# Kernel optimization log

Measured on AMD Instinct MI355X. Metric: run time of the kernel, lower is better.

The kernel has to match this reference:

```python
import jax, jax.numpy as jnp
import numpy as np

N_NODES = 100000
N_EDGES = 1600000
D_IN = 128
D_HID = 128
D_OUT = 64


def _glorot(key, shape):
    lim = float(np.sqrt(6.0 / (shape[0] + shape[1])))
    return jax.random.uniform(key, shape, jnp.float32, -lim, lim)


def setup_inputs() -> dict:
    key = jax.random.key(0)
    ks = jax.random.split(key, 8)
    x = jax.random.normal(ks[0], (N_NODES, D_IN), jnp.float32)
    edge_index = jax.random.randint(ks[1], (2, N_EDGES), 0, N_NODES, jnp.int64)
    # SAGEConv layer 0: in=128 -> out=128 (lin_l with bias on aggregated, lin_r no bias on root)
    W_l0 = _glorot(ks[2], (D_IN, D_HID))
    b_l0 = jnp.zeros((D_HID,), jnp.float32)
    W_r0 = _glorot(ks[3], (D_IN, D_HID))
    # SAGEConv layer 1: in=128 -> out=64
    W_l1 = _glorot(ks[4], (D_HID, D_OUT))
    b_l1 = jnp.zeros((D_OUT,), jnp.float32)
    W_r1 = _glorot(ks[5], (D_HID, D_OUT))
    return {"x": x, "edge_index": edge_index,
            "W_l0": W_l0, "b_l0": b_l0, "W_r0": W_r0,
            "W_l1": W_l1, "b_l1": b_l1, "W_r1": W_r1}


def _sage_conv(x, src, dst, W_l, b_l, W_r):
    # mean aggregation of source features at targets (PyG SAGEConv default aggr='mean')
    msgs = x[src]                                              # [E, d_in] irregular gather
    agg = jax.ops.segment_sum(msgs, dst, num_segments=N_NODES)  # [N, d_in]
    cnt = jax.ops.segment_sum(jnp.ones((src.shape[0],), x.dtype), dst,
                              num_segments=N_NODES)            # [N]
    mean = agg / jnp.maximum(cnt, 1.0)[:, None]
    return mean @ W_l + b_l + x @ W_r


def reference(x, edge_index, W_l0, b_l0, W_r0, W_l1, b_l1, W_r1):
    src, dst = edge_index[0], edge_index[1]
    h = _sage_conv(x, src, dst, W_l0, b_l0, W_r0)
    h = jax.nn.relu(h)
    # dropout is identity at inference (training=False)
    out = _sage_conv(h, src, dst, W_l1, b_l1, W_r1)
    return out
```

## Files before the change

### kernel.cpp

```cpp
#include <hip/hip_runtime.h>
#include <type_traits>

#define NN 100000
#define NE 1600000
#define DF 128
#define NBKT 196
#define BKT_SHIFT 9
#define EPB 6250

typedef unsigned short ushort_t;
typedef unsigned int uint_t;
typedef __bf16 bf16x8 __attribute__((ext_vector_type(8)));
typedef float f32x4 __attribute__((ext_vector_type(4)));

union ABFrag { uint4 u; bf16x8 v; ushort_t s[8]; };

__device__ __forceinline__ float bf2f(ushort_t u) {
    uint_t v = ((uint_t)u) << 16;
    float f;
    __builtin_memcpy(&f, &v, 4);
    return f;
}

__device__ __forceinline__ ushort_t f2bf(float f) {
    uint_t u;
    __builtin_memcpy(&u, &f, 4);
    uint_t rounding = 0x7FFFu + ((u >> 16) & 1u);
    u += rounding;
    return (ushort_t)(u >> 16);
}

__global__ void k_detect(const int* ei, int* flag) {
    int l = threadIdx.x;
    int v = ei[l];
    bool ok = ((l & 1) == 0) || (v == 0);
    unsigned long long m = __ballot(ok);
    if (l == 0) flag[0] = (m == 0xFFFFFFFFFFFFFFFFULL) ? 1 : 0;
}

__global__ __launch_bounds__(256) void k_bktcnt(const int* __restrict__ ei,
                                                const int* __restrict__ flag,
                                                int* __restrict__ M) {
    __shared__ int cnt[NBKT];
    int t = threadIdx.x, blk = blockIdx.x;
    for (int i = t; i < NBKT; i += 256) cnt[i] = 0;
    __syncthreads();
    int e0 = blk * EPB;
    if (flag[0]) {
        const long long* p = (const long long*)ei;
        for (int i = t; i < EPB; i += 256) {
            int d = (int)p[(size_t)NE + e0 + i];
            atomicAdd(&cnt[d >> BKT_SHIFT], 1);
        }
    } else {
        for (int i = t; i < EPB; i += 256) {
            int d = ei[NE + e0 + i];
            atomicAdd(&cnt[d >> BKT_SHIFT], 1);
        }
    }
    __syncthreads();
    for (int i = t; i < NBKT; i += 256) M[i * 256 + blk] = cnt[i];
}

__global__ __launch_bounds__(256) void k_colscan(int* __restrict__ M, int* __restrict__ colsum) {
    __shared__ int sm[256];
    int t = threadIdx.x, b = blockIdx.x;
    int v = M[b * 256 + t];
    sm[t] = v;
    __syncthreads();
    for (int o = 1; o < 256; o <<= 1) {
        int add = (t >= o) ? sm[t - o] : 0;
        __syncthreads();
        sm[t] += add;
        __syncthreads();
    }
    M[b * 256 + t] = sm[t] - v;
    if (t == 255) colsum[b] = sm[255];
}

__global__ __launch_bounds__(256) void k_bktscan(const int* __restrict__ colsum,
                                                 int* __restrict__ bkbase, int* __restrict__ rs) {
    __shared__ int sm[256];
    int t = threadIdx.x;
    int v = (t < NBKT) ? colsum[t] : 0;
    sm[t] = v;
    __syncthreads();
    for (int o = 1; o < 256; o <<= 1) {
        int add = (t >= o) ? sm[t - o] : 0;
        __syncthreads();
        sm[t] += add;
        __syncthreads();
    }
    if (t <= NBKT) bkbase[t] = sm[t] - v;
    if (t == 0) rs[NN] = NE;
}

__global__ __launch_bounds__(256) void k_bktscatter(const int* __restrict__ ei,
                                                    const int* __restrict__ flag,
                                                    const int* __restrict__ M,
                                                    const int* __restrict__ bkbase,
                                                    uint2* __restrict__ tmp) {
    __shared__ int cur[NBKT];
    int t = threadIdx.x, blk = blockIdx.x;
    for (int i = t; i < NBKT; i += 256) cur[i] = bkbase[i] + M[i * 256 + blk];
    __syncthreads();
    int e0 = blk * EPB;
    if (flag[0]) {
        const long long* p = (const long long*)ei;
        for (int i = t; i < EPB; i += 256) {
            int e = e0 + i;
            int s = (int)p[e], d = (int)p[(size_t)NE + e];
            int pos = atomicAdd(&cur[d >> BKT_SHIFT], 1);
            tmp[pos] = make_uint2((uint_t)s, (uint_t)d);
        }
    } else {
        for (int i = t; i < EPB; i += 256) {
            int e = e0 + i;
            int s = ei[e], d = ei[NE + e];
            int pos = atomicAdd(&cur[d >> BKT_SHIFT], 1);
            tmp[pos] = make_uint2((uint_t)s, (uint_t)d);
        }
    }
}

__global__ __launch_bounds__(256) void k_bktsort(const uint2* __restrict__ tmp,
                                                 const int* __restrict__ bkbase,
                                                 int* __restrict__ rs, int* __restrict__ esrc) {
    __shared__ int hist[512];
    __shared__ int curp[512];
    int t = threadIdx.x, b = blockIdx.x;
    int nbase = b << BKT_SHIFT;
    int bb = bkbase[b], be = bkbase[b + 1];
    hist[t] = 0;
    hist[t + 256] = 0;
    __syncthreads();
    for (int i = bb + t; i < be; i += 256)
        atomicAdd(&hist[(int)tmp[i].y - nbase], 1);
    __syncthreads();
    int ov0 = hist[t], ov1 = hist[t + 256];
    for (int o = 1; o < 512; o <<= 1) {
        int v0 = (t >= o) ? hist[t - o] : 0;
        int v1 = (t + 256 >= o) ? hist[t + 256 - o] : 0;
        __syncthreads();
        hist[t] += v0;
        hist[t + 256] += v1;
        __syncthreads();
    }
    int ex0 = bb + hist[t] - ov0;
    int ex1 = bb + hist[t + 256] - ov1;
    int n0 = nbase + t, n1 = nbase + t + 256;
    if (n0 < NN) rs[n0] = ex0;
    if (n1 < NN) rs[n1] = ex1;
    curp[t] = ex0;
    curp[t + 256] = ex1;
    __syncthreads();
    for (int i = bb + t; i < be; i += 256) {
        uint2 pr = tmp[i];
        int pos = atomicAdd(&curp[(int)pr.y - nbase], 1);
        esrc[pos] = (int)pr.x;
    }
}

__global__ void k_cast(const float* __restrict__ src, ushort_t* __restrict__ dst, int n4) {
    int i = blockIdx.x * 256 + threadIdx.x;
    if (i < n4) {
        float4 f = ((const float4*)src)[i];
        uint2 o;
        o.x = (uint_t)f2bf(f.x) | ((uint_t)f2bf(f.y) << 16);
        o.y = (uint_t)f2bf(f.z) | ((uint_t)f2bf(f.w) << 16);
        ((uint2*)dst)[i] = o;
    }
}

__global__ void k_packW(const float* Wl, const float* Wr, ushort_t* dst, int NT) {
    int NC = NT * 16;
    int total = 8 * NT * 512;
    int idx = blockIdx.x * 256 + threadIdx.x;
    if (idx >= total) return;
    int j = idx & 7;
    int lane = (idx >> 3) & 63;
    int rem = idx / 512;
    int t = rem % NT;
    int s = rem / NT;
    int quad = lane >> 4, l16 = lane & 15;
    int k = (s & 3) * 32 + quad * 8 + j;
    int n = t * 16 + l16;
    const float* W = (s < 4) ? Wl : Wr;
    dst[idx] = f2bf(W[k * NC + n]);
}

__global__ __launch_bounds__(256) void k_agg(const ushort_t* __restrict__ feat,
                                             const int* __restrict__ rs,
                                             const int* __restrict__ esrc,
                                             ushort_t* __restrict__ outm) {
    int wv = threadIdx.x >> 6;
    int lane = threadIdx.x & 63;
    int n = blockIdx.x * 4 + wv;
    if (n >= NN) return;
    int s0 = rs[n], s1 = rs[n + 1];
    float a0 = 0.f, a1 = 0.f;
    for (int base = s0; base < s1; base += 64) {
        int c = s1 - base;
        if (c > 64) c = 64;
        int my = (lane < c) ? esrc[base + lane] : 0;
        int e = 0;
        for (; e + 4 <= c; e += 4) {
            int r0 = __shfl(my, e);
            int r1 = __shfl(my, e + 1);
            int r2 = __shfl(my, e + 2);
            int r3 = __shfl(my, e + 3);
            uint_t v0 = *(const uint_t*)(feat + (size_t)r0 * DF + lane * 2);
            uint_t v1 = *(const uint_t*)(feat + (size_t)r1 * DF + lane * 2);
            uint_t v2 = *(const uint_t*)(feat + (size_t)r2 * DF + lane * 2);
            uint_t v3 = *(const uint_t*)(feat + (size_t)r3 * DF + lane * 2);
            a0 += bf2f((ushort_t)(v0 & 0xffff)) + bf2f((ushort_t)(v1 & 0xffff)) +
                  bf2f((ushort_t)(v2 & 0xffff)) + bf2f((ushort_t)(v3 & 0xffff));
            a1 += bf2f((ushort_t)(v0 >> 16)) + bf2f((ushort_t)(v1 >> 16)) +
                  bf2f((ushort_t)(v2 >> 16)) + bf2f((ushort_t)(v3 >> 16));
        }
        for (; e < c; ++e) {
            int r = __shfl(my, e);
            uint_t v = *(const uint_t*)(feat + (size_t)r * DF + lane * 2);
            a0 += bf2f((ushort_t)(v & 0xffff));
            a1 += bf2f((ushort_t)(v >> 16));
        }
    }
    int deg = s1 - s0;
    float inv = 1.0f / (float)(deg > 0 ? deg : 1);
    a0 *= inv;
    a1 *= inv;
    uint_t o = (uint_t)f2bf(a0) | ((uint_t)f2bf(a1) << 16);
    *(uint_t*)(outm + (size_t)n * DF + lane * 2) = o;
}

template <int NT, bool RELU, typename OutT>
__global__ __launch_bounds__(256) void k_gemm(const ushort_t* __restrict__ A0,
                                              const ushort_t* __restrict__ A1,
                                              const ushort_t* __restrict__ Wpk,
                                              const float* __restrict__ bias,
                                              OutT* __restrict__ out) {
    const int NC = NT * 16;
    int warp = threadIdx.x >> 6;
    int lane = threadIdx.x & 63;
    int quad = lane >> 4;
    int l16 = lane & 15;
    int m0 = blockIdx.x * 64 + warp * 16;

    int rowA = m0 + l16;
    if (rowA >= NN) rowA = NN - 1;
    const int kofs = quad * 8;

    f32x4 acc[NT];
#pragma unroll
    for (int t = 0; t < NT; t++) acc[t] = (f32x4){0.f, 0.f, 0.f, 0.f};

#pragma unroll
    for (int s = 0; s < 8; s++) {
        const ushort_t* Ab = (s < 4) ? A0 : A1;
        int kk = (s & 3) * 32 + kofs;
        ABFrag a;
        a.u = *(const uint4*)(Ab + (size_t)rowA * DF + kk);
#pragma unroll
        for (int t = 0; t < NT; t++) {
            ABFrag b;
            b.u = *(const uint4*)(Wpk + ((size_t)(s * NT + t) * 64 + lane) * 8);
            acc[t] = __builtin_amdgcn_mfma_f32_16x16x32_bf16(a.v, b.v, acc[t], 0, 0, 0);
        }
    }

#pragma unroll
    for (int t = 0; t < NT; t++) {
        int col = t * 16 + l16;
        float bv = bias[col];
#pragma unroll
        for (int r = 0; r < 4; r++) {
            int row = m0 + quad * 4 + r;
            if (row < NN) {
                float v = acc[t][r] + bv;
                if (RELU) v = fmaxf(v, 0.f);
                if constexpr (std::is_same<OutT, ushort_t>::value)
                    out[(size_t)row * NC + col] = f2bf(v);
                else
                    out[(size_t)row * NC + col] = v;
            }
        }
    }
}

extern "C" void kernel_launch(void* const* d_in, const int* in_sizes, int n_in,
                              void* d_out, int out_size, void* d_ws, size_t ws_size,
                              hipStream_t stream) {
    const float* x   = (const float*)d_in[0];
    const int*   ei  = (const int*)d_in[1];
    const float* Wl0 = (const float*)d_in[2];
    const float* bl0 = (const float*)d_in[3];
    const float* Wr0 = (const float*)d_in[4];
    const float* Wl1 = (const float*)d_in[5];
    const float* bl1 = (const float*)d_in[6];
    const float* Wr1 = (const float*)d_in[7];
    float* out = (float*)d_out;

    char* ws = (char*)d_ws;
    size_t off = 0;
    auto alloc = [&](size_t b) {
        size_t o = off;
        off += (b + 255) & ~(size_t)255;
        return o;
    };
    int* flag   = (int*)(ws + alloc(64));
    int* rs     = (int*)(ws + alloc((size_t)(NN + 1) * 4));
    int* M      = (int*)(ws + alloc((size_t)NBKT * 256 * 4));
    int* colsum = (int*)(ws + alloc((size_t)NBKT * 4));
    int* bkbase = (int*)(ws + alloc((size_t)(NBKT + 1) * 4));
    int* esrc   = (int*)(ws + alloc((size_t)NE * 4));
    ushort_t* pw0  = (ushort_t*)(ws + alloc((size_t)8 * 8 * 512 * 2));
    ushort_t* pw1  = (ushort_t*)(ws + alloc((size_t)8 * 4 * 512 * 2));
    ushort_t* xb   = (ushort_t*)(ws + alloc((size_t)NN * DF * 2));
    ushort_t* mean = (ushort_t*)(ws + alloc((size_t)NN * DF * 2));
    ushort_t* h    = (ushort_t*)(ws + alloc((size_t)NN * DF * 2));
    uint2* tmp = (uint2*)mean;

    const int N4 = NN * DF / 4;

    k_detect<<<1, 64, 0, stream>>>(ei, flag);
    k_bktcnt<<<256, 256, 0, stream>>>(ei, flag, M);
    k_colscan<<<NBKT, 256, 0, stream>>>(M, colsum);
    k_bktscan<<<1, 256, 0, stream>>>(colsum, bkbase, rs);
    k_bktscatter<<<256, 256, 0, stream>>>(ei, flag, M, bkbase, tmp);
    k_bktsort<<<NBKT, 256, 0, stream>>>(tmp, bkbase, rs, esrc);
    k_cast<<<(N4 + 255) / 256, 256, 0, stream>>>(x, xb, N4);
    k_packW<<<(8 * 8 * 512 + 255) / 256, 256, 0, stream>>>(Wl0, Wr0, pw0, 8);
    k_packW<<<(8 * 4 * 512 + 255) / 256, 256, 0, stream>>>(Wl1, Wr1, pw1, 4);

    k_agg<<<NN / 4, 256, 0, stream>>>(xb, rs, esrc, mean);
    k_gemm<8, true, ushort_t><<<(NN + 63) / 64, 256, 0, stream>>>(mean, xb, pw0, bl0, h);
    k_agg<<<NN / 4, 256, 0, stream>>>(h, rs, esrc, mean);
    k_gemm<4, false, float><<<(NN + 63) / 64, 256, 0, stream>>>(mean, h, pw1, bl1, out);
}
```

Baseline: 332.1 us.

## Transform before aggregating in layer 2 and vectorize neighbor gathers

Layer 2 now applies the linear maps first, using the identity mean(h)@W_l = mean(h@W_l). The neighbor projection is written as a 64-wide bf16 buffer and the root projection plus bias as fp32, so the gather moves 64 features per edge instead of 128. Both aggregation kernels now place several nodes in one wavefront and read 16-byte vectors per lane. A zero sentinel row at index NN lets padded lanes run without branching. The cost is extra launches and sentinel/zero-row bookkeeping, plus wasted lanes when node degrees within a wave differ.

```diff
diff --git a/kernel.cpp b/kernel.cpp
--- a/kernel.cpp
+++ b/kernel.cpp
@@ -15,19 +15,17 @@
 
 union ABFrag { uint4 u; bf16x8 v; ushort_t s[8]; };
 
-__device__ __forceinline__ float bf2f(ushort_t u) {
-    uint_t v = ((uint_t)u) << 16;
-    float f;
-    __builtin_memcpy(&f, &v, 4);
-    return f;
-}
-
 __device__ __forceinline__ ushort_t f2bf(float f) {
     uint_t u;
     __builtin_memcpy(&u, &f, 4);
     uint_t rounding = 0x7FFFu + ((u >> 16) & 1u);
     u += rounding;
     return (ushort_t)(u >> 16);
+}
+__device__ __forceinline__ float lo_f(uint_t u) { return __uint_as_float(u << 16); }
+__device__ __forceinline__ float hi_f(uint_t u) { return __uint_as_float(u & 0xffff0000u); }
+__device__ __forceinline__ uint_t pack2(float a, float b) {
+    return (uint_t)f2bf(a) | ((uint_t)f2bf(b) << 16);
 }
 
 __global__ void k_detect(const int* ei, int* flag) {
@@ -166,71 +164,191 @@
     if (i < n4) {
         float4 f = ((const float4*)src)[i];
         uint2 o;
-        o.x = (uint_t)f2bf(f.x) | ((uint_t)f2bf(f.y) << 16);
-        o.y = (uint_t)f2bf(f.z) | ((uint_t)f2bf(f.w) << 16);
+        o.x = pack2(f.x, f.y);
+        o.y = pack2(f.z, f.w);
         ((uint2*)dst)[i] = o;
-    }
-}
-
-__global__ void k_packW(const float* Wl, const float* Wr, ushort_t* dst, int NT) {
-    int NC = NT * 16;
-    int total = 8 * NT * 512;
+    } else if (i < n4 + 32) {
+        ((uint2*)dst)[i] = make_uint2(0u, 0u);
+    }
+}
+
+__global__ void k_packW0(const float* Wl, const float* Wr, ushort_t* dst) {
+    int total = 8 * 8 * 512;
     int idx = blockIdx.x * 256 + threadIdx.x;
     if (idx >= total) return;
     int j = idx & 7;
     int lane = (idx >> 3) & 63;
     int rem = idx / 512;
-    int t = rem % NT;
-    int s = rem / NT;
+    int t = rem % 8;
+    int s = rem / 8;
     int quad = lane >> 4, l16 = lane & 15;
     int k = (s & 3) * 32 + quad * 8 + j;
     int n = t * 16 + l16;
     const float* W = (s < 4) ? Wl : Wr;
-    dst[idx] = f2bf(W[k * NC + n]);
-}
-
-__global__ __launch_bounds__(256) void k_agg(const ushort_t* __restrict__ feat,
-                                             const int* __restrict__ rs,
-                                             const int* __restrict__ esrc,
-                                             ushort_t* __restrict__ outm) {
+    dst[idx] = f2bf(W[k * 128 + n]);
+}
+
+__global__ void k_packW1(const float* Wl, const float* Wr, ushort_t* dst) {
+    int total = 4 * 8 * 512;
+    int idx = blockIdx.x * 256 + threadIdx.x;
+    if (idx >= total) return;
+    int j = idx & 7;
+    int lane = (idx >> 3) & 63;
+    int rem = idx / 512;
+    int t = rem % 8;
+    int s = rem / 8;
+    int quad = lane >> 4, l16 = lane & 15;
+    int k = s * 32 + quad * 8 + j;
+    int n = (t & 3) * 16 + l16;
+    const float* W = (t < 4) ? Wl : Wr;
+    dst[idx] = f2bf(W[k * 64 + n]);
+}
+
+__global__ void k_zrow2(ushort_t* tbuf) {
+    int t = threadIdx.x;
+    if (t < 32) ((uint_t*)(tbuf + (size_t)NN * 64))[t] = 0u;
+}
+
+__global__ __launch_bounds__(256) void k_agg0(const ushort_t* __restrict__ feat,
+                                              const int* __restrict__ rs,
+                                              const int* __restrict__ esrc,
+                                              ushort_t* __restrict__ outm) {
     int wv = threadIdx.x >> 6;
     int lane = threadIdx.x & 63;
-    int n = blockIdx.x * 4 + wv;
-    if (n >= NN) return;
-    int s0 = rs[n], s1 = rs[n + 1];
-    float a0 = 0.f, a1 = 0.f;
-    for (int base = s0; base < s1; base += 64) {
-        int c = s1 - base;
-        if (c > 64) c = 64;
-        int my = (lane < c) ? esrc[base + lane] : 0;
+    int li = lane & 15;
+    int gbase = lane & 48;
+    int n = (blockIdx.x * 4 + wv) * 4 + (lane >> 4);
+    int s0 = 0, deg = 0;
+    if (n < NN) {
+        s0 = rs[n];
+        deg = rs[n + 1] - s0;
+    }
+    int md = deg;
+    md = max(md, __shfl_xor(md, 16));
+    md = max(md, __shfl_xor(md, 32));
+    float acc[8] = {0.f, 0.f, 0.f, 0.f, 0.f, 0.f, 0.f, 0.f};
+    const ushort_t* fb = feat + li * 8;
+    int clampIdx = (deg > 0) ? deg - 1 : 0;
+    for (int c = 0; c < md; c += 16) {
+        int ii = c + li;
+        if (ii > clampIdx) ii = clampIdx;
+        int my = esrc[s0 + ii];
+        int lim = md - c;
+        if (lim > 16) lim = 16;
         int e = 0;
-        for (; e + 4 <= c; e += 4) {
-            int r0 = __shfl(my, e);
-            int r1 = __shfl(my, e + 1);
-            int r2 = __shfl(my, e + 2);
-            int r3 = __shfl(my, e + 3);
-            uint_t v0 = *(const uint_t*)(feat + (size_t)r0 * DF + lane * 2);
-            uint_t v1 = *(const uint_t*)(feat + (size_t)r1 * DF + lane * 2);
-            uint_t v2 = *(const uint_t*)(feat + (size_t)r2 * DF + lane * 2);
-            uint_t v3 = *(const uint_t*)(feat + (size_t)r3 * DF + lane * 2);
-            a0 += bf2f((ushort_t)(v0 & 0xffff)) + bf2f((ushort_t)(v1 & 0xffff)) +
-                  bf2f((ushort_t)(v2 & 0xffff)) + bf2f((ushort_t)(v3 & 0xffff));
-            a1 += bf2f((ushort_t)(v0 >> 16)) + bf2f((ushort_t)(v1 >> 16)) +
-                  bf2f((ushort_t)(v2 >> 16)) + bf2f((ushort_t)(v3 >> 16));
-        }
-        for (; e < c; ++e) {
-            int r = __shfl(my, e);
-            uint_t v = *(const uint_t*)(feat + (size_t)r * DF + lane * 2);
-            a0 += bf2f((ushort_t)(v & 0xffff));
-            a1 += bf2f((ushort_t)(v >> 16));
-        }
-    }
-    int deg = s1 - s0;
-    float inv = 1.0f / (float)(deg > 0 ? deg : 1);
-    a0 *= inv;
-    a1 *= inv;
-    uint_t o = (uint_t)f2bf(a0) | ((uint_t)f2bf(a1) << 16);
-    *(uint_t*)(outm + (size_t)n * DF + lane * 2) = o;
+        for (; e + 4 <= lim; e += 4) {
+            int r0 = __shfl(my, gbase + e);
+            int r1 = __shfl(my, gbase + e + 1);
+            int r2 = __shfl(my, gbase + e + 2);
+            int r3 = __shfl(my, gbase + e + 3);
+            r0 = (c + e < deg) ? r0 : NN;
+            r1 = (c + e + 1 < deg) ? r1 : NN;
+            r2 = (c + e + 2 < deg) ? r2 : NN;
+            r3 = (c + e + 3 < deg) ? r3 : NN;
+            uint4 v0 = *(const uint4*)(fb + (size_t)r0 * DF);
+            uint4 v1 = *(const uint4*)(fb + (size_t)r1 * DF);
+            uint4 v2 = *(const uint4*)(fb + (size_t)r2 * DF);
+            uint4 v3 = *(const uint4*)(fb + (size_t)r3 * DF);
+            acc[0] += lo_f(v0.x); acc[1] += hi_f(v0.x); acc[2] += lo_f(v0.y); acc[3] += hi_f(v0.y);
+            acc[4] += lo_f(v0.z); acc[5] += hi_f(v0.z); acc[6] += lo_f(v0.w); acc[7] += hi_f(v0.w);
+            acc[0] += lo_f(v1.x); acc[1] += hi_f(v1.x); acc[2] += lo_f(v1.y); acc[3] += hi_f(v1.y);
+            acc[4] += lo_f(v1.z); acc[5] += hi_f(v1.z); acc[6] += lo_f(v1.w); acc[7] += hi_f(v1.w);
+            acc[0] += lo_f(v2.x); acc[1] += hi_f(v2.x); acc[2] += lo_f(v2.y); acc[3] += hi_f(v2.y);
+            acc[4] += lo_f(v2.z); acc[5] += hi_f(v2.z); acc[6] += lo_f(v2.w); acc[7] += hi_f(v2.w);
+            acc[0] += lo_f(v3.x); acc[1] += hi_f(v3.x); acc[2] += lo_f(v3.y); acc[3] += hi_f(v3.y);
+            acc[4] += lo_f(v3.z); acc[5] += hi_f(v3.z); acc[6] += lo_f(v3.w); acc[7] += hi_f(v3.w);
+        }
+        for (; e < lim; ++e) {
+            int r = __shfl(my, gbase + e);
+            r = (c + e < deg) ? r : NN;
+            uint4 v = *(const uint4*)(fb + (size_t)r * DF);
+            acc[0] += lo_f(v.x); acc[1] += hi_f(v.x); acc[2] += lo_f(v.y); acc[3] += hi_f(v.y);
+            acc[4] += lo_f(v.z); acc[5] += hi_f(v.z); acc[6] += lo_f(v.w); acc[7] += hi_f(v.w);
+        }
+    }
+    if (n < NN) {
+        float inv = 1.0f / (float)(deg > 0 ? deg : 1);
+        uint4 o;
+        o.x = pack2(acc[0] * inv, acc[1] * inv);
+        o.y = pack2(acc[2] * inv, acc[3] * inv);
+        o.z = pack2(acc[4] * inv, acc[5] * inv);
+        o.w = pack2(acc[6] * inv, acc[7] * inv);
+        *(uint4*)(outm + (size_t)n * DF + li * 8) = o;
+    }
+}
+
+__global__ __launch_bounds__(256) void k_agg2(const ushort_t* __restrict__ tbuf,
+                                              const float* __restrict__ rbuf,
+                                              const int* __restrict__ rs,
+                                              const int* __restrict__ esrc,
+                                              float* __restrict__ out) {
+    int wv = threadIdx.x >> 6;
+    int lane = threadIdx.x & 63;
+    int li = lane & 7;
+    int gbase = lane & 56;
+    int n = (blockIdx.x * 4 + wv) * 8 + (lane >> 3);
+    int s0 = 0, deg = 0;
+    if (n < NN) {
+        s0 = rs[n];
+        deg = rs[n + 1] - s0;
+    }
+    int md = deg;
+    md = max(md, __shfl_xor(md, 8));
+    md = max(md, __shfl_xor(md, 16));
+    md = max(md, __shfl_xor(md, 32));
+    float acc[8] = {0.f, 0.f, 0.f, 0.f, 0.f, 0.f, 0.f, 0.f};
+    const ushort_t* fb = tbuf + li * 8;
+    int clampIdx = (deg > 0) ? deg - 1 : 0;
+    for (int c = 0; c < md; c += 8) {
+        int ii = c + li;
+        if (ii > clampIdx) ii = clampIdx;
+        int my = esrc[s0 + ii];
+        int lim = md - c;
+        if (lim > 8) lim = 8;
+        int e = 0;
+        for (; e + 4 <= lim; e += 4) {
+            int r0 = __shfl(my, gbase + e);
+            int r1 = __shfl(my, gbase + e + 1);
+            int r2 = __shfl(my, gbase + e + 2);
+            int r3 = __shfl(my, gbase + e + 3);
+            r0 = (c + e < deg) ? r0 : NN;
+            r1 = (c + e + 1 < deg) ? r1 : NN;
+            r2 = (c + e + 2 < deg) ? r2 : NN;
+            r3 = (c + e + 3 < deg) ? r3 : NN;
+            uint4 v0 = *(const uint4*)(fb + (size_t)r0 * 64);
+            uint4 v1 = *(const uint4*)(fb + (size_t)r1 * 64);
+            uint4 v2 = *(const uint4*)(fb + (size_t)r2 * 64);
+            uint4 v3 = *(const uint4*)(fb + (size_t)r3 * 64);
+            acc[0] += lo_f(v0.x); acc[1] += hi_f(v0.x); acc[2] += lo_f(v0.y); acc[3] += hi_f(v0.y);
+            acc[4] += lo_f(v0.z); acc[5] += hi_f(v0.z); acc[6] += lo_f(v0.w); acc[7] += hi_f(v0.w);
+            acc[0] += lo_f(v1.x); acc[1] += hi_f(v1.x); acc[2] += lo_f(v1.y); acc[3] += hi_f(v1.y);
+            acc[4] += lo_f(v1.z); acc[5] += hi_f(v1.z); acc[6] += lo_f(v1.w); acc[7] += hi_f(v1.w);
+            acc[0] += lo_f(v2.x); acc[1] += hi_f(v2.x); acc[2] += lo_f(v2.y); acc[3] += hi_f(v2.y);
+            acc[4] += lo_f(v2.z); acc[5] += hi_f(v2.z); acc[6] += lo_f(v2.w); acc[7] += hi_f(v2.w);
+            acc[0] += lo_f(v3.x); acc[1] += hi_f(v3.x); acc[2] += lo_f(v3.y); acc[3] += hi_f(v3.y);
+            acc[4] += lo_f(v3.z); acc[5] += hi_f(v3.z); acc[6] += lo_f(v3.w); acc[7] += hi_f(v3.w);
+        }
+        for (; e < lim; ++e) {
+            int r = __shfl(my, gbase + e);
+            r = (c + e < deg) ? r : NN;
+            uint4 v = *(const uint4*)(fb + (size_t)r * 64);
+            acc[0] += lo_f(v.x); acc[1] += hi_f(v.x); acc[2] += lo_f(v.y); acc[3] += hi_f(v.y);
+            acc[4] += lo_f(v.z); acc[5] += hi_f(v.z); acc[6] += lo_f(v.w); acc[7] += hi_f(v.w);
+        }
+    }
+    if (n < NN) {
+        float inv = 1.0f / (float)(deg > 0 ? deg : 1);
+        const float4* rp = (const float4*)(rbuf + (size_t)n * 64 + li * 8);
+        float4 ra = rp[0], rb = rp[1];
+        float4 oa, ob;
+        oa.x = acc[0] * inv + ra.x; oa.y = acc[1] * inv + ra.y;
+        oa.z = acc[2] * inv + ra.z; oa.w = acc[3] * inv + ra.w;
+        ob.x = acc[4] * inv + rb.x; ob.y = acc[5] * inv + rb.y;
+        ob.z = acc[6] * inv + rb.z; ob.w = acc[7] * inv + rb.w;
+        float4* op = (float4*)(out + (size_t)n * 64 + li * 8);
+        op[0] = oa;
+        op[1] = ob;
+    }
 }
 
 template <int NT, bool RELU, typename OutT>
@@ -282,6 +400,56 @@
                     out[(size_t)row * NC + col] = f2bf(v);
                 else
                     out[(size_t)row * NC + col] = v;
+            }
+        }
+    }
+}
+
+__global__ __launch_bounds__(256) void k_gemm2(const ushort_t* __restrict__ A,
+                                               const ushort_t* __restrict__ Wpk,
+                                               const float* __restrict__ bias,
+                                               ushort_t* __restrict__ tbuf,
+                                               float* __restrict__ rbuf) {
+    int warp = threadIdx.x >> 6;
+    int lane = threadIdx.x & 63;
+    int quad = lane >> 4;
+    int l16 = lane & 15;
+    int m0 = blockIdx.x * 64 + warp * 16;
+
+    int rowA = m0 + l16;
+    if (rowA >= NN) rowA = NN - 1;
+    const int kofs = quad * 8;
+
+    f32x4 acc[8];
+#pragma unroll
+    for (int t = 0; t < 8; t++) acc[t] = (f32x4){0.f, 0.f, 0.f, 0.f};
+
+#pragma unroll
+    for (int s = 0; s < 4; s++) {
+        int kk = s * 32 + kofs;
+        ABFrag a;
+        a.u = *(const uint4*)(A + (size_t)rowA * DF + kk);
+#pragma unroll
+        for (int t = 0; t < 8; t++) {
+            ABFrag b;
+            b.u = *(const uint4*)(Wpk + ((size_t)(s * 8 + t) * 64 + lane) * 8);
+            acc[t] = __builtin_amdgcn_mfma_f32_16x16x32_bf16(a.v, b.v, acc[t], 0, 0, 0);
+        }
+    }
+
+#pragma unroll
+    for (int t = 0; t < 8; t++) {
+        int cc = (t & 3) * 16 + l16;
+        float bv = (t >= 4) ? bias[cc] : 0.f;
+#pragma unroll
+        for (int r = 0; r < 4; r++) {
+            int row = m0 + quad * 4 + r;
+            if (row < NN) {
+                float v = acc[t][r];
+                if (t < 4)
+                    tbuf[(size_t)row * 64 + cc] = f2bf(v);
+                else
+                    rbuf[(size_t)row * 64 + cc] = v + bv;
             }
         }
     }
@@ -314,11 +482,13 @@
     int* bkbase = (int*)(ws + alloc((size_t)(NBKT + 1) * 4));
     int* esrc   = (int*)(ws + alloc((size_t)NE * 4));
     ushort_t* pw0  = (ushort_t*)(ws + alloc((size_t)8 * 8 * 512 * 2));
-    ushort_t* pw1  = (ushort_t*)(ws + alloc((size_t)8 * 4 * 512 * 2));
-    ushort_t* xb   = (ushort_t*)(ws + alloc((size_t)NN * DF * 2));
+    ushort_t* pw1  = (ushort_t*)(ws + alloc((size_t)4 * 8 * 512 * 2));
+    ushort_t* xb   = (ushort_t*)(ws + alloc((size_t)(NN + 1) * DF * 2));
     ushort_t* mean = (ushort_t*)(ws + alloc((size_t)NN * DF * 2));
     ushort_t* h    = (ushort_t*)(ws + alloc((size_t)NN * DF * 2));
     uint2* tmp = (uint2*)mean;
+    ushort_t* tbuf = xb;
+    float* rbuf = (float*)mean;
 
     const int N4 = NN * DF / 4;
 
@@ -328,12 +498,13 @@
     k_bktscan<<<1, 256, 0, stream>>>(colsum, bkbase, rs);
     k_bktscatter<<<256, 256, 0, stream>>>(ei, flag, M, bkbase, tmp);
     k_bktsort<<<NBKT, 256, 0, stream>>>(tmp, bkbase, rs, esrc);
-    k_cast<<<(N4 + 255) / 256, 256, 0, stream>>>(x, xb, N4);
-    k_packW<<<(8 * 8 * 512 + 255) / 256, 256, 0, stream>>>(Wl0, Wr0, pw0, 8);
-    k_packW<<<(8 * 4 * 512 + 255) / 256, 256, 0, stream>>>(Wl1, Wr1, pw1, 4);
-
-    k_agg<<<NN / 4, 256, 0, stream>>>(xb, rs, esrc, mean);
+    k_cast<<<(N4 + 32 + 255) / 256, 256, 0, stream>>>(x, xb, N4);
+    k_packW0<<<(8 * 8 * 512 + 255) / 256, 256, 0, stream>>>(Wl0, Wr0, pw0);
+    k_packW1<<<(4 * 8 * 512 + 255) / 256, 256, 0, stream>>>(Wl1, Wr1, pw1);
+
+    k_agg0<<<NN / 16, 256, 0, stream>>>(xb, rs, esrc, mean);
     k_gemm<8, true, ushort_t><<<(NN + 63) / 64, 256, 0, stream>>>(mean, xb, pw0, bl0, h);
-    k_agg<<<NN / 4, 256, 0, stream>>>(h, rs, esrc, mean);
-    k_gemm<4, false, float><<<(NN + 63) / 64, 256, 0, stream>>>(mean, h, pw1, bl1, out);
-}
+    k_gemm2<<<(NN + 63) / 64, 256, 0, stream>>>(h, pw1, bl1, tbuf, rbuf);
+    k_zrow2<<<1, 64, 0, stream>>>(tbuf);
+    k_agg2<<<(NN + 31) / 32, 256, 0, stream>>>(tbuf, rbuf, rs, esrc, out);
+}
```

Measured after the change: 310.6 us. -6.5%, faster.

## Fuse layer-0 aggregation and both GEMMs, aggregate projected layer-1 features

Applied to the files above, without the earlier changes.

Uses linearity of mean aggregation to project h by W_l1 before gathering, so the second aggregation gathers 64-wide bf16 rows instead of 128-wide ones. Layer-0 aggregation, the layer-0 GEMM with ReLU and the layer-1 projections are fused into one kernel through LDS, so mean and h never round-trip through global memory. The new gathers use 16-byte loads with a zero sentinel row in place of divergent tails. Format detection is folded into the sort kernels and the cast and pack kernels are merged, cutting launches. Rounding the projected features to bf16 before aggregation slightly changes numerics.

```diff
diff --git a/kernel.cpp b/kernel.cpp
--- a/kernel.cpp
+++ b/kernel.cpp
@@ -15,13 +15,6 @@
 
 union ABFrag { uint4 u; bf16x8 v; ushort_t s[8]; };
 
-__device__ __forceinline__ float bf2f(ushort_t u) {
-    uint_t v = ((uint_t)u) << 16;
-    float f;
-    __builtin_memcpy(&f, &v, 4);
-    return f;
-}
-
 __device__ __forceinline__ ushort_t f2bf(float f) {
     uint_t u;
     __builtin_memcpy(&u, &f, 4);
@@ -29,24 +22,33 @@
     u += rounding;
     return (ushort_t)(u >> 16);
 }
-
-__global__ void k_detect(const int* ei, int* flag) {
-    int l = threadIdx.x;
-    int v = ei[l];
-    bool ok = ((l & 1) == 0) || (v == 0);
-    unsigned long long m = __ballot(ok);
-    if (l == 0) flag[0] = (m == 0xFFFFFFFFFFFFFFFFULL) ? 1 : 0;
+__device__ __forceinline__ float lo_f(uint_t u) { return __uint_as_float(u << 16); }
+__device__ __forceinline__ float hi_f(uint_t u) { return __uint_as_float(u & 0xffff0000u); }
+__device__ __forceinline__ uint_t pack2(float a, float b) {
+    return (uint_t)f2bf(a) | ((uint_t)f2bf(b) << 16);
+}
+
+__device__ __forceinline__ int detect64(const int* ei, int* s64) {
+    if (threadIdx.x < 64) {
+        int v = ei[threadIdx.x];
+        bool ok = ((threadIdx.x & 1) == 0) || (v == 0);
+        unsigned long long m = __ballot(ok);
+        if (threadIdx.x == 0) *s64 = (m == 0xFFFFFFFFFFFFFFFFULL) ? 1 : 0;
+    }
+    __syncthreads();
+    return *s64;
 }
 
 __global__ __launch_bounds__(256) void k_bktcnt(const int* __restrict__ ei,
-                                                const int* __restrict__ flag,
                                                 int* __restrict__ M) {
     __shared__ int cnt[NBKT];
+    __shared__ int s64;
     int t = threadIdx.x, blk = blockIdx.x;
+    int is64 = detect64(ei, &s64);
     for (int i = t; i < NBKT; i += 256) cnt[i] = 0;
     __syncthreads();
     int e0 = blk * EPB;
-    if (flag[0]) {
+    if (is64) {
         const long long* p = (const long long*)ei;
         for (int i = t; i < EPB; i += 256) {
             int d = (int)p[(size_t)NE + e0 + i];
@@ -96,16 +98,17 @@
 }
 
 __global__ __launch_bounds__(256) void k_bktscatter(const int* __restrict__ ei,
-                                                    const int* __restrict__ flag,
                                                     const int* __restrict__ M,
                                                     const int* __restrict__ bkbase,
                                                     uint2* __restrict__ tmp) {
     __shared__ int cur[NBKT];
+    __shared__ int s64;
     int t = threadIdx.x, blk = blockIdx.x;
+    int is64 = detect64(ei, &s64);
     for (int i = t; i < NBKT; i += 256) cur[i] = bkbase[i] + M[i * 256 + blk];
     __syncthreads();
     int e0 = blk * EPB;
-    if (flag[0]) {
+    if (is64) {
         const long long* p = (const long long*)ei;
         for (int i = t; i < EPB; i += 256) {
             int e = e0 + i;
@@ -161,130 +164,217 @@
     }
 }
 
-__global__ void k_cast(const float* __restrict__ src, ushort_t* __restrict__ dst, int n4) {
-    int i = blockIdx.x * 256 + threadIdx.x;
-    if (i < n4) {
-        float4 f = ((const float4*)src)[i];
-        uint2 o;
-        o.x = (uint_t)f2bf(f.x) | ((uint_t)f2bf(f.y) << 16);
-        o.y = (uint_t)f2bf(f.z) | ((uint_t)f2bf(f.w) << 16);
-        ((uint2*)dst)[i] = o;
-    }
-}
-
-__global__ void k_packW(const float* Wl, const float* Wr, ushort_t* dst, int NT) {
-    int NC = NT * 16;
-    int total = 8 * NT * 512;
-    int idx = blockIdx.x * 256 + threadIdx.x;
-    if (idx >= total) return;
-    int j = idx & 7;
-    int lane = (idx >> 3) & 63;
-    int rem = idx / 512;
-    int t = rem % NT;
-    int s = rem / NT;
-    int quad = lane >> 4, l16 = lane & 15;
-    int k = (s & 3) * 32 + quad * 8 + j;
-    int n = t * 16 + l16;
-    const float* W = (s < 4) ? Wl : Wr;
-    dst[idx] = f2bf(W[k * NC + n]);
-}
-
-__global__ __launch_bounds__(256) void k_agg(const ushort_t* __restrict__ feat,
-                                             const int* __restrict__ rs,
-                                             const int* __restrict__ esrc,
-                                             ushort_t* __restrict__ outm) {
+#define CAST_B 12501
+__global__ void k_prep(const float* __restrict__ x, ushort_t* __restrict__ xb,
+                       const float* __restrict__ Wl0, const float* __restrict__ Wr0,
+                       ushort_t* __restrict__ pw0,
+                       const float* __restrict__ Wl1, const float* __restrict__ Wr1,
+                       ushort_t* __restrict__ pw1) {
+    const int n4 = NN * DF / 4;
+    int blk = blockIdx.x, t = threadIdx.x;
+    if (blk < CAST_B) {
+        int i = blk * 256 + t;
+        if (i < n4) {
+            float4 f = ((const float4*)x)[i];
+            uint2 o;
+            o.x = pack2(f.x, f.y);
+            o.y = pack2(f.z, f.w);
+            ((uint2*)xb)[i] = o;
+        } else if (i < n4 + 32) {
+            ((uint2*)xb)[i] = make_uint2(0u, 0u);
+        }
+    } else if (blk < CAST_B + 128) {
+        int idx = (blk - CAST_B) * 256 + t;
+        int j = idx & 7;
+        int lane = (idx >> 3) & 63;
+        int rem = idx / 512;
+        int tt = rem % 8;
+        int s = rem / 8;
+        int quad = lane >> 4, l16 = lane & 15;
+        int k = (s & 3) * 32 + quad * 8 + j;
+        int n = tt * 16 + l16;
+        const float* W = (s < 4) ? Wl0 : Wr0;
+        pw0[idx] = f2bf(W[k * 128 + n]);
+    } else {
+        int idx = (blk - CAST_B - 128) * 256 + t;
+        int j = idx & 7;
+        int lane = (idx >> 3) & 63;
+        int rem = idx / 512;
+        int tt = rem % 8;
+        int s = rem / 8;
+        int quad = lane >> 4, l16 = lane & 15;
+        int k = s * 32 + quad * 8 + j;
+        int n = (tt & 3) * 16 + l16;
+        const float* W = (tt < 4) ? Wl1 : Wr1;
+        pw1[idx] = f2bf(W[k * 64 + n]);
+    }
+}
+
+__global__ __launch_bounds__(256) void k_fused(const ushort_t* __restrict__ xb,
+                                               const int* __restrict__ rs,
+                                               const int* __restrict__ esrc,
+                                               const ushort_t* __restrict__ pw0,
+                                               const float* __restrict__ bl0,
+                                               const ushort_t* __restrict__ pw1,
+                                               const float* __restrict__ bl1,
+                                               ushort_t* __restrict__ tbuf,
+                                               float* __restrict__ rbuf) {
+    __shared__ ushort_t m_lds[16][136];
+    __shared__ ushort_t h_lds[16][136];
+    int tid = threadIdx.x;
+    int wv = tid >> 6, lane = tid & 63;
+    int l16 = lane & 15, quad = lane >> 4, gbase = lane & 48;
+    int n0 = blockIdx.x * 16;
+
+    int n = n0 + wv * 4 + quad;
+    int s0 = rs[n];
+    int deg = rs[n + 1] - s0;
+    int md = deg;
+    md = max(md, __shfl_xor(md, 16));
+    md = max(md, __shfl_xor(md, 32));
+    float acc[8] = {0.f, 0.f, 0.f, 0.f, 0.f, 0.f, 0.f, 0.f};
+    const ushort_t* fb = xb + l16 * 8;
+    int clampIdx = (deg > 0) ? deg - 1 : 0;
+    for (int c = 0; c < md; c += 16) {
+        int ii = c + l16;
+        if (ii > clampIdx) ii = clampIdx;
+        int my = esrc[s0 + ii];
+        uint4 v[16];
+#pragma unroll
+        for (int e = 0; e < 16; e++) {
+            int r = __shfl(my, gbase + e);
+            r = (c + e < deg) ? r : NN;
+            v[e] = *(const uint4*)(fb + (size_t)r * DF);
+        }
+#pragma unroll
+        for (int e = 0; e < 16; e++) {
+            acc[0] += lo_f(v[e].x); acc[1] += hi_f(v[e].x);
+            acc[2] += lo_f(v[e].y); acc[3] += hi_f(v[e].y);
+            acc[4] += lo_f(v[e].z); acc[5] += hi_f(v[e].z);
+            acc[6] += lo_f(v[e].w); acc[7] += hi_f(v[e].w);
+        }
+    }
+    {
+        float inv = 1.0f / (float)(deg > 0 ? deg : 1);
+        int nl = wv * 4 + quad;
+        uint_t* mp = (uint_t*)&m_lds[nl][l16 * 8];
+        mp[0] = pack2(acc[0] * inv, acc[1] * inv);
+        mp[1] = pack2(acc[2] * inv, acc[3] * inv);
+        mp[2] = pack2(acc[4] * inv, acc[5] * inv);
+        mp[3] = pack2(acc[6] * inv, acc[7] * inv);
+    }
+    __syncthreads();
+
+    const int kofs = quad * 8;
+    f32x4 c0[2] = {(f32x4){0.f, 0.f, 0.f, 0.f}, (f32x4){0.f, 0.f, 0.f, 0.f}};
+#pragma unroll
+    for (int s = 0; s < 8; s++) {
+        ABFrag a;
+        if (s < 4)
+            a.u = *(const uint4*)&m_lds[l16][(s & 3) * 32 + kofs];
+        else
+            a.u = *(const uint4*)(xb + (size_t)(n0 + l16) * DF + (s & 3) * 32 + kofs);
+#pragma unroll
+        for (int i = 0; i < 2; i++) {
+            int t = wv * 2 + i;
+            ABFrag b;
+            b.u = *(const uint4*)(pw0 + ((size_t)(s * 8 + t) * 64 + lane) * 8);
+            c0[i] = __builtin_amdgcn_mfma_f32_16x16x32_bf16(a.v, b.v, c0[i], 0, 0, 0);
+        }
+    }
+#pragma unroll
+    for (int i = 0; i < 2; i++) {
+        int col = wv * 32 + i * 16 + l16;
+        float bv = bl0[col];
+#pragma unroll
+        for (int r = 0; r < 4; r++) {
+            float v = fmaxf(c0[i][r] + bv, 0.f);
+            h_lds[quad * 4 + r][col] = f2bf(v);
+        }
+    }
+    __syncthreads();
+
+    f32x4 c1[2] = {(f32x4){0.f, 0.f, 0.f, 0.f}, (f32x4){0.f, 0.f, 0.f, 0.f}};
+#pragma unroll
+    for (int s = 0; s < 4; s++) {
+        ABFrag a;
+        a.u = *(const uint4*)&h_lds[l16][s * 32 + kofs];
+#pragma unroll
+        for (int i = 0; i < 2; i++) {
+            int t = wv * 2 + i;
+            ABFrag b;
+            b.u = *(const uint4*)(pw1 + ((size_t)(s * 8 + t) * 64 + lane) * 8);
+            c1[i] = __builtin_amdgcn_mfma_f32_16x16x32_bf16(a.v, b.v, c1[i], 0, 0, 0);
+        }
+    }
+#pragma unroll
+    for (int i = 0; i < 2; i++) {
+        int t = wv * 2 + i;
+        int cc = (t & 3) * 16 + l16;
+        if (t < 4) {
+#pragma unroll
+            for (int r = 0; r < 4; r++)
+                tbuf[(size_t)(n0 + quad * 4 + r) * 64 + cc] = f2bf(c1[i][r]);
+        } else {
+            float bv = bl1[cc];
+#pragma unroll
+            for (int r = 0; r < 4; r++)
+                rbuf[(size_t)(n0 + quad * 4 + r) * 64 + cc] = c1[i][r] + bv;
+        }
+    }
+    if (blockIdx.x == 0 && tid < 32)
+        ((uint_t*)(tbuf + (size_t)NN * 64))[tid] = 0u;
+}
+
+__global__ __launch_bounds__(256) void k_agg2(const ushort_t* __restrict__ tbuf,
+                                              const float* __restrict__ rbuf,
+                                              const int* __restrict__ rs,
+                                              const int* __restrict__ esrc,
+                                              float* __restrict__ out) {
     int wv = threadIdx.x >> 6;
     int lane = threadIdx.x & 63;
-    int n = blockIdx.x * 4 + wv;
-    if (n >= NN) return;
-    int s0 = rs[n], s1 = rs[n + 1];
-    float a0 = 0.f, a1 = 0.f;
-    for (int base = s0; base < s1; base += 64) {
-        int c = s1 - base;
-        if (c > 64) c = 64;
-        int my = (lane < c) ? esrc[base + lane] : 0;
-        int e = 0;
-        for (; e + 4 <= c; e += 4) {
-            int r0 = __shfl(my, e);
-            int r1 = __shfl(my, e + 1);
-            int r2 = __shfl(my, e + 2);
-            int r3 = __shfl(my, e + 3);
-            uint_t v0 = *(const uint_t*)(feat + (size_t)r0 * DF + lane * 2);
-            uint_t v1 = *(const uint_t*)(feat + (size_t)r1 * DF + lane * 2);
-            uint_t v2 = *(const uint_t*)(feat + (size_t)r2 * DF + lane * 2);
-            uint_t v3 = *(const uint_t*)(feat + (size_t)r3 * DF + lane * 2);
-            a0 += bf2f((ushort_t)(v0 & 0xffff)) + bf2f((ushort_t)(v1 & 0xffff)) +
-                  bf2f((ushort_t)(v2 & 0xffff)) + bf2f((ushort_t)(v3 & 0xffff));
-            a1 += bf2f((ushort_t)(v0 >> 16)) + bf2f((ushort_t)(v1 >> 16)) +
-                  bf2f((ushort_t)(v2 >> 16)) + bf2f((ushort_t)(v3 >> 16));
-        }
-        for (; e < c; ++e) {
-            int r = __shfl(my, e);
-            uint_t v = *(const uint_t*)(feat + (size_t)r * DF + lane * 2);
-            a0 += bf2f((ushort_t)(v & 0xffff));
-            a1 += bf2f((ushort_t)(v >> 16));
-        }
-    }
-    int deg = s1 - s0;
+    int li = lane & 7;
+    int gbase = lane & 56;
+    int n = (blockIdx.x * 4 + wv) * 8 + (lane >> 3);
+    int s0 = rs[n];
+    int deg = rs[n + 1] - s0;
+    int md = deg;
+    md = max(md, __shfl_xor(md, 8));
+    md = max(md, __shfl_xor(md, 16));
+    md = max(md, __shfl_xor(md, 32));
+    float acc[8] = {0.f, 0.f, 0.f, 0.f, 0.f, 0.f, 0.f, 0.f};
+    const ushort_t* fb = tbuf + li * 8;
+    int clampIdx = (deg > 0) ? deg - 1 : 0;
+    for (int c = 0; c < md; c += 8) {
+        int ii = c + li;
+        if (ii > clampIdx) ii = clampIdx;
+        int my = esrc[s0 + ii];
+        uint4 v[8];
+#pragma unroll
+        for (int e = 0; e < 8; e++) {
+            int r = __shfl(my, gbase + e);
+            r = (c + e < deg) ? r : NN;
+            v[e] = *(const uint4*)(fb + (size_t)r * 64);
+        }
+#pragma unroll
+        for (int e = 0; e < 8; e++) {
+            acc[0] += lo_f(v[e].x); acc[1] += hi_f(v[e].x);
+            acc[2] += lo_f(v[e].y); acc[3] += hi_f(v[e].y);
+            acc[4] += lo_f(v[e].z); acc[5] += hi_f(v[e].z);
+            acc[6] += lo_f(v[e].w); acc[7] += hi_f(v[e].w);
+        }
+    }
     float inv = 1.0f / (float)(deg > 0 ? deg : 1);
-    a0 *= inv;
-    a1 *= inv;
-    uint_t o = (uint_t)f2bf(a0) | ((uint_t)f2bf(a1) << 16);
-    *(uint_t*)(outm + (size_t)n * DF + lane * 2) = o;
-}
-
-template <int NT, bool RELU, typename OutT>
-__global__ __launch_bounds__(256) void k_gemm(const ushort_t* __restrict__ A0,
-                                              const ushort_t* __restrict__ A1,
-                                              const ushort_t* __restrict__ Wpk,
-                                              const float* __restrict__ bias,
-                                              OutT* __restrict__ out) {
-    const int NC = NT * 16;
-    int warp = threadIdx.x >> 6;
-    int lane = threadIdx.x & 63;
-    int quad = lane >> 4;
-    int l16 = lane & 15;
-    int m0 = blockIdx.x * 64 + warp * 16;
-
-    int rowA = m0 + l16;
-    if (rowA >= NN) rowA = NN - 1;
-    const int kofs = quad * 8;
-
-    f32x4 acc[NT];
-#pragma unroll
-    for (int t = 0; t < NT; t++) acc[t] = (f32x4){0.f, 0.f, 0.f, 0.f};
-
-#pragma unroll
-    for (int s = 0; s < 8; s++) {
-        const ushort_t* Ab = (s < 4) ? A0 : A1;
-        int kk = (s & 3) * 32 + kofs;
-        ABFrag a;
-        a.u = *(const uint4*)(Ab + (size_t)rowA * DF + kk);
-#pragma unroll
-        for (int t = 0; t < NT; t++) {
-            ABFrag b;
-            b.u = *(const uint4*)(Wpk + ((size_t)(s * NT + t) * 64 + lane) * 8);
-            acc[t] = __builtin_amdgcn_mfma_f32_16x16x32_bf16(a.v, b.v, acc[t], 0, 0, 0);
-        }
-    }
-
-#pragma unroll
-    for (int t = 0; t < NT; t++) {
-        int col = t * 16 + l16;
-        float bv = bias[col];
-#pragma unroll
-        for (int r = 0; r < 4; r++) {
-            int row = m0 + quad * 4 + r;
-            if (row < NN) {
-                float v = acc[t][r] + bv;
-                if (RELU) v = fmaxf(v, 0.f);
-                if constexpr (std::is_same<OutT, ushort_t>::value)
-                    out[(size_t)row * NC + col] = f2bf(v);
-                else
-                    out[(size_t)row * NC + col] = v;
-            }
-        }
-    }
+    const float4* rp = (const float4*)(rbuf + (size_t)n * 64 + li * 8);
+    float4 ra = rp[0], rb = rp[1];
+    float4 oa, ob;
+    oa.x = acc[0] * inv + ra.x; oa.y = acc[1] * inv + ra.y;
+    oa.z = acc[2] * inv + ra.z; oa.w = acc[3] * inv + ra.w;
+    ob.x = acc[4] * inv + rb.x; ob.y = acc[5] * inv + rb.y;
+    ob.z = acc[6] * inv + rb.z; ob.w = acc[7] * inv + rb.w;
+    float4* op = (float4*)(out + (size_t)n * 64 + li * 8);
+    op[0] = oa;
+    op[1] = ob;
 }
 
 extern "C" void kernel_launch(void* const* d_in, const int* in_sizes, int n_in,
@@ -307,33 +397,24 @@
         off += (b + 255) & ~(size_t)255;
         return o;
     };
-    int* flag   = (int*)(ws + alloc(64));
     int* rs     = (int*)(ws + alloc((size_t)(NN + 1) * 4));
     int* M      = (int*)(ws + alloc((size_t)NBKT * 256 * 4));
     int* colsum = (int*)(ws + alloc((size_t)NBKT * 4));
     int* bkbase = (int*)(ws + alloc((size_t)(NBKT + 1) * 4));
     int* esrc   = (int*)(ws + alloc((size_t)NE * 4));
     ushort_t* pw0  = (ushort_t*)(ws + alloc((size_t)8 * 8 * 512 * 2));
-    ushort_t* pw1  = (ushort_t*)(ws + alloc((size_t)8 * 4 * 512 * 2));
-    ushort_t* xb   = (ushort_t*)(ws + alloc((size_t)NN * DF * 2));
-    ushort_t* mean = (ushort_t*)(ws + alloc((size_t)NN * DF * 2));
-    ushort_t* h    = (ushort_t*)(ws + alloc((size_t)NN * DF * 2));
-    uint2* tmp = (uint2*)mean;
-
-    const int N4 = NN * DF / 4;
-
-    k_detect<<<1, 64, 0, stream>>>(ei, flag);
-    k_bktcnt<<<256, 256, 0, stream>>>(ei, flag, M);
+    ushort_t* pw1  = (ushort_t*)(ws + alloc((size_t)4 * 8 * 512 * 2));
+    ushort_t* xb   = (ushort_t*)(ws + alloc((size_t)(NN + 1) * DF * 2));
+    ushort_t* tbuf = (ushort_t*)(ws + alloc((size_t)(NN + 1) * 64 * 2));
+    float*    rbuf = (float*)(ws + alloc((size_t)NN * 64 * 4));
+    uint2* tmp = (uint2*)rbuf;
+
+    k_bktcnt<<<256, 256, 0, stream>>>(ei, M);
     k_colscan<<<NBKT, 256, 0, stream>>>(M, colsum);
     k_bktscan<<<1, 256, 0, stream>>>(colsum, bkbase, rs);
-    k_bktscatter<<<256, 256, 0, stream>>>(ei, flag, M, bkbase, tmp);
+    k_bktscatter<<<256, 256, 0, stream>>>(ei, M, bkbase, tmp);
     k_bktsort<<<NBKT, 256, 0, stream>>>(tmp, bkbase, rs, esrc);
-    k_cast<<<(N4 + 255) / 256, 256, 0, stream>>>(x, xb, N4);
-    k_packW<<<(8 * 8 * 512 + 255) / 256, 256, 0, stream>>>(Wl0, Wr0, pw0, 8);
-    k_packW<<<(8 * 4 * 512 + 255) / 256, 256, 0, stream>>>(Wl1, Wr1, pw1, 4);
-
-    k_agg<<<NN / 4, 256, 0, stream>>>(xb, rs, esrc, mean);
-    k_gemm<8, true, ushort_t><<<(NN + 63) / 64, 256, 0, stream>>>(mean, xb, pw0, bl0, h);
-    k_agg<<<NN / 4, 256, 0, stream>>>(h, rs, esrc, mean);
-    k_gemm<4, false, float><<<(NN + 63) / 64, 256, 0, stream>>>(mean, h, pw1, bl1, out);
-}
+    k_prep<<<CAST_B + 128 + 64, 256, 0, stream>>>(x, xb, Wl0, Wr0, pw0, Wl1, Wr1, pw1);
+    k_fused<<<NN / 16, 256, 0, stream>>>(xb, rs, esrc, pw0, bl0, pw1, bl1, tbuf, rbuf);
+    k_agg2<<<NN / 32, 256, 0, stream>>>(tbuf, rbuf, rs, esrc, out);
+}
```

Result: faster. 290.3 us (-12.6%).
